# Kernel tuning notes

Measured on AMD Instinct MI355X. Metric: run time of the kernel, lower is better.

The kernel has to match this reference:

```python
import jax, jax.numpy as jnp
import numpy as np

NUM_BUCKETS = 32
MAX_DISTANCE = 128
NUM_HEADS = 16
D_KV = 64


def _relative_position_bucket(relative_position):
    # bidirectional buckets, faithful to T5Attention._relative_position_bucket
    num_buckets = NUM_BUCKETS // 2
    relative_buckets = (relative_position > 0).astype(jnp.int32) * num_buckets
    relative_position = jnp.abs(relative_position)
    max_exact = num_buckets // 2
    is_small = relative_position < max_exact
    rp_f = relative_position.astype(jnp.float32)
    rel_if_large = max_exact + (
        jnp.log(rp_f / max_exact) / np.log(MAX_DISTANCE / max_exact) * (num_buckets - max_exact)
    )
    rel_if_large = jnp.minimum(rel_if_large, num_buckets - 1)
    relative_buckets = relative_buckets + jnp.where(is_small, rp_f, rel_if_large).astype(jnp.int32)
    return relative_buckets


def setup_inputs() -> dict:
    key = jax.random.key(0)
    ks = jax.random.split(key, 6)
    B, S, D = 2, 2048, 1024
    inner = NUM_HEADS * D_KV  # 1024
    q_std = (inner * D_KV) ** (-0.5)
    kv_std = inner ** (-0.5)
    return {
        "hidden_states": jax.random.normal(ks[0], (B, S, D), jnp.float32),
        "attention_mask": jnp.ones((B, S), jnp.int32),
        "Wq": jax.random.normal(ks[1], (D, inner), jnp.float32) * q_std,
        "Wk": jax.random.normal(ks[2], (D, inner), jnp.float32) * kv_std,
        "Wv": jax.random.normal(ks[3], (D, inner), jnp.float32) * kv_std,
        "Wo": jax.random.normal(ks[4], (inner, D), jnp.float32) * kv_std,
        "rel_bias": jax.random.normal(ks[5], (NUM_BUCKETS, NUM_HEADS), jnp.float32),
    }


def reference(hidden_states, attention_mask, Wq, Wk, Wv, Wo, rel_bias):
    B, S, D = hidden_states.shape
    H, Dk = NUM_HEADS, D_KV

    q = (hidden_states @ Wq).reshape(B, S, H, Dk)
    k = (hidden_states @ Wk).reshape(B, S, H, Dk)
    v = (hidden_states @ Wv).reshape(B, S, H, Dk)
    q = q / jnp.sqrt(jnp.asarray(Dk, q.dtype))

    scores = jnp.einsum('bthd,bshd->bhts', q, k)  # [B,H,S,S]

    # relative position bias
    pos = jnp.arange(S, dtype=jnp.int32)
    rel_pos = pos[None, :] - pos[:, None]          # memory - context, [S,S]
    buckets = _relative_position_bucket(rel_pos)   # [S,S]
    bias = rel_bias[buckets]                       # [S,S,H]
    scores = scores + bias.transpose(2, 0, 1)[None].astype(scores.dtype)

    mask = attention_mask[:, None, None, :].astype(scores.dtype)
    scores = scores + (1.0 - mask) * jnp.finfo(scores.dtype).min

    attn = jax.nn.softmax(scores, axis=-1)
    out = jnp.einsum('bhts,bshd->bthd', attn, v).reshape(B, S, H * Dk)
    return out @ Wo
```

## Files before the change

kernel.cpp:

```cpp
#include <hip/hip_runtime.h>
#include <hip/hip_bf16.h>
#include <math.h>

typedef __attribute__((ext_vector_type(8))) short bf16x8;
typedef __attribute__((ext_vector_type(4))) short s16x4;
typedef __attribute__((ext_vector_type(4))) float f32x4;

constexpr int cB = 2, cS = 2048, cH = 16, cD = 64, cIn = 1024, cM = 1024;
constexpr float cLog2e = 1.4426950408889634f;

union BfPack { bf16x8 v; short s[8]; };
union BfPack4 { s16x4 v; short s[4]; };

__device__ __forceinline__ short f2bf(float f) {
    union { float f; unsigned u; } v; v.f = f;
    unsigned r = v.u + 0x7fffu + ((v.u >> 16) & 1u);
    return (short)(r >> 16);
}

__device__ __forceinline__ f32x4 mfma16(bf16x8 a, bf16x8 b, f32x4 c) {
    return __builtin_amdgcn_mfma_f32_16x16x32_bf16(a, b, c, 0, 0, 0);
}

__device__ __forceinline__ void async16(const short* g, short* l) {
    __builtin_amdgcn_global_load_lds(
        (const __attribute__((address_space(1))) unsigned*)(uintptr_t)g,
        (__attribute__((address_space(3))) unsigned*)(uintptr_t)l, 16, 0, 0);
}

__global__ __launch_bounds__(256) void prep_kernel(
    const float* __restrict__ hidden, short* __restrict__ hbf,
    const float* __restrict__ Wq, const float* __restrict__ Wk,
    const float* __restrict__ Wv, const float* __restrict__ Wo,
    short* __restrict__ Wt,
    const float* __restrict__ rel_bias, const int* __restrict__ mask,
    float* __restrict__ bt, float* __restrict__ maskadd) {
    const int bid = blockIdx.x;
    const int tid = threadIdx.x;
    if (bid < 2048) {
        int t = bid * 256 + tid;
        const float4* src = (const float4*)hidden;
        float4 a = src[2 * t], b = src[2 * t + 1];
        BfPack p;
        p.s[0] = f2bf(a.x); p.s[1] = f2bf(a.y); p.s[2] = f2bf(a.z); p.s[3] = f2bf(a.w);
        p.s[4] = f2bf(b.x); p.s[5] = f2bf(b.y); p.s[6] = f2bf(b.z); p.s[7] = f2bf(b.w);
        ((bf16x8*)hbf)[t] = p.v;
    } else if (bid < 3072) {
        const int b2 = bid - 2048;
        const int z = b2 >> 8, rem = b2 & 255;
        const float* W = (z == 0) ? Wq : (z == 1) ? Wk : (z == 2) ? Wv : Wo;
        const float scale = (z == 0) ? 0.125f * cLog2e : 1.0f;
        const int n0 = (rem & 15) * 64, k0 = (rem >> 4) * 64;
        __shared__ short sW[64][72];
        const int r = tid >> 2, c4 = (tid & 3) * 16;
        {
            const float* src = W + (size_t)(k0 + r) * cM + n0 + c4;
            BfPack p[2];
            #pragma unroll
            for (int q = 0; q < 2; q++) {
                float4 x = ((const float4*)src)[2 * q];
                float4 y = ((const float4*)src)[2 * q + 1];
                p[q].s[0] = f2bf(x.x * scale); p[q].s[1] = f2bf(x.y * scale);
                p[q].s[2] = f2bf(x.z * scale); p[q].s[3] = f2bf(x.w * scale);
                p[q].s[4] = f2bf(y.x * scale); p[q].s[5] = f2bf(y.y * scale);
                p[q].s[6] = f2bf(y.z * scale); p[q].s[7] = f2bf(y.w * scale);
            }
            *(bf16x8*)&sW[r][c4] = p[0].v;
            *(bf16x8*)&sW[r][c4 + 8] = p[1].v;
        }
        __syncthreads();
        const int n = tid >> 2, kc = (tid & 3) * 16;
        BfPack o0, o1;
        #pragma unroll
        for (int j = 0; j < 8; j++) o0.s[j] = sW[kc + j][n];
        #pragma unroll
        for (int j = 0; j < 8; j++) o1.s[j] = sW[kc + 8 + j][n];
        short* dst = Wt + (size_t)z * cM * cIn + (size_t)(n0 + n) * cIn + k0 + kc;
        *(bf16x8*)dst = o0.v;
        *(bf16x8*)(dst + 8) = o1.v;
    } else {
        int idx = (bid - 3072) * 256 + tid;
        if (idx < 4096) maskadd[idx] = (1.0f - (float)mask[idx]) * -3.0e38f;
        if (idx >= 4095) return;
        int delta = idx - 2047;
        int rb = (delta > 0) ? 16 : 0;
        int ar = delta < 0 ? -delta : delta;
        int bucket;
        if (ar < 8) {
            bucket = rb + ar;
        } else {
            float rl = 8.0f + logf((float)ar * 0.125f) * 2.8853900817779268f;
            rl = fminf(rl, 15.0f);
            bucket = rb + (int)rl;
        }
        #pragma unroll
        for (int h = 0; h < cH; h++)
            bt[h * 4096 + 2048 + delta] = rel_bias[bucket * cH + h] * cLog2e;
    }
}

template <bool SWAP>
__device__ __forceinline__ void gemm_core(
    const short* __restrict__ A, const short* __restrict__ Bt,
    short* smem, int m0, int c0, int tid, f32x4 (&acc)[4][4]) {
    const int w = tid >> 6, l = tid & 63;
    const int m16 = l & 15, g = l >> 4;
    const int srow = l >> 2, scol = (l & 3) * 8;
    const int mq = (w & 1) * 64, nq = (w >> 1) * 64;

    const short* pA0 = A + (size_t)(m0 + w * 16 + srow) * cIn + scol;
    const short* pA1 = A + (size_t)(m0 + 64 + w * 16 + srow) * cIn + scol;
    const short* pB0 = Bt + (size_t)(c0 + w * 16 + srow) * cIn + scol;
    const short* pB1 = Bt + (size_t)(c0 + 64 + w * 16 + srow) * cIn + scol;
    const int dof = w * 512 + l * 8;

    async16(pA0, smem + dof);
    async16(pA1, smem + 2048 + dof);
    async16(pB0, smem + 4096 + dof);
    async16(pB1, smem + 6144 + dof);
    __syncthreads();

    for (int k0 = 0; k0 < cIn; k0 += 32) {
        const int buf = (k0 >> 5) & 1;
        if (k0 + 32 < cIn) {
            short* dn = smem + (buf ^ 1) * 8192 + dof;
            async16(pA0 + k0 + 32, dn);
            async16(pA1 + k0 + 32, dn + 2048);
            async16(pB0 + k0 + 32, dn + 4096);
            async16(pB1 + k0 + 32, dn + 6144);
        }
        const short* sA = smem + buf * 8192;
        const short* sB = sA + 4096;
        bf16x8 af[4], bf[4];
        #pragma unroll
        for (int i = 0; i < 4; i++)
            af[i] = *(const bf16x8*)(sA + (mq + i * 16 + m16) * 32 + g * 8);
        #pragma unroll
        for (int j = 0; j < 4; j++)
            bf[j] = *(const bf16x8*)(sB + (nq + j * 16 + m16) * 32 + g * 8);
        #pragma unroll
        for (int i = 0; i < 4; i++)
            #pragma unroll
            for (int j = 0; j < 4; j++)
                acc[i][j] = SWAP ? mfma16(bf[j], af[i], acc[i][j])
                                 : mfma16(af[i], bf[j], acc[i][j]);
        __syncthreads();
    }
}

__global__ __launch_bounds__(256) void gemm_qkv_kernel(
    const short* __restrict__ hbf, const short* __restrict__ Wt,
    short* __restrict__ Qrm, short* __restrict__ Krm, short* __restrict__ VT) {
    const int raw = blockIdx.x;
    const int xcd = raw & 7;
    const int rest = raw >> 3;
    const int cblk = rest & 7;
    const int t = rest >> 3;
    const int z = t >> 2;
    const int m0 = (xcd * 4 + (t & 3)) * 128;
    const int c0 = cblk * 128;

    const short* Bt = Wt + (size_t)z * cM * cIn;
    __shared__ short smem[128 * 132];
    const int tid = threadIdx.x, w = tid >> 6, l = tid & 63;
    const int m16 = l & 15, g = l >> 4;
    const int mq = (w & 1) * 64, nq = (w >> 1) * 64;
    f32x4 acc[4][4] = {};

    if (z <= 1) {
        gemm_core<false>(hbf, Bt, smem, m0, c0, tid, acc);
        __syncthreads();
        #pragma unroll
        for (int i = 0; i < 4; i++)
            #pragma unroll
            for (int j = 0; j < 4; j++)
                #pragma unroll
                for (int r = 0; r < 4; r++)
                    smem[(mq + i * 16 + g * 4 + r) * 132 + nq + j * 16 + m16] =
                        f2bf(acc[i][j][r]);
        __syncthreads();
        const int tr = tid >> 1, hf = (tid & 1) * 64;
        short* dst = ((z == 0) ? Qrm : Krm) + (size_t)(m0 + tr) * cM + c0 + hf;
        #pragma unroll
        for (int c = 0; c < 8; c++)
            *(bf16x8*)(dst + c * 8) = *(const bf16x8*)(smem + tr * 132 + hf + c * 8);
    } else {
        gemm_core<true>(hbf, Bt, smem, m0, c0, tid, acc);
        __syncthreads();
        #pragma unroll
        for (int i = 0; i < 4; i++) {
            const int sl = mq + i * 16 + m16;
            const int s6 = sl & 63;
            const int pcol = (sl & 64) +
                             ((s6 & 3) | ((s6 & 28) << 1) | ((s6 >> 3) & 4));
            #pragma unroll
            for (int j = 0; j < 4; j++)
                #pragma unroll
                for (int r = 0; r < 4; r++)
                    smem[(nq + j * 16 + g * 4 + r) * 132 + pcol] =
                        f2bf(acc[i][j][r]);
        }
        __syncthreads();
        const int tr = tid >> 1, hf = (tid & 1) * 64;
        const int wcol = c0 + tr;
        short* dst = VT + (((size_t)(m0 >> 11) * cH + (wcol >> 6)) * cD +
                           (wcol & 63)) * cS + (m0 & 2047) + hf;
        #pragma unroll
        for (int c = 0; c < 8; c++)
            *(bf16x8*)(dst + c * 8) = *(const bf16x8*)(smem + tr * 132 + hf + c * 8);
    }
}

__global__ __launch_bounds__(512, 1) void attn_kernel(
    const short* __restrict__ Qrm, const short* __restrict__ Krm,
    const short* __restrict__ VTK, const float* __restrict__ maskadd,
    const float* __restrict__ bias_t, short* __restrict__ ctx) {
    const int raw = blockIdx.x;
    const int xcd = raw & 7, j = raw >> 3;
    const int qi = j & 7, grp = j >> 3;
    const int bh = grp * 8 + xcd;
    const int b = bh >> 4, h = bh & 15;
    const int q0 = qi * 256;

    const short* VTp = VTK + ((size_t)b * cH + h) * cS * cD;
    const float* mp = maskadd + b * cS;

    const int tid = threadIdx.x;
    const int wave = tid >> 6, lane = tid & 63;
    const int m16 = lane & 15, g = lane >> 4;

    __shared__ short Kt[2][128 * 64];
    __shared__ short Vt[2][64 * 128];
    __shared__ float bias_lds[2304];

    {
        const float* bw = bias_t + h * 4096 + 2048 - (q0 + 255);
        for (int i = tid; i < 2303; i += 512)
            bias_lds[i] = bw[i];
    }

    int qv[2];
    bf16x8 qf[2][2];
    #pragma unroll
    for (int qq = 0; qq < 2; qq++) {
        qv[qq] = q0 + wave * 16 + qq * 128 + m16;
        const short* qb = Qrm + (size_t)(b * cS + qv[qq]) * cM + h * cD;
        qf[qq][0] = *(const bf16x8*)(qb + g * 8);
        qf[qq][1] = *(const bf16x8*)(qb + 32 + g * 8);
    }

    int ib[2];
    #pragma unroll
    for (int qq = 0; qq < 2; qq++)
        ib[qq] = q0 + 255 + g * 4 - qv[qq];

    f32x4 o[2][4] = {};
    f32x4 lacc[2] = {};
    BfPack ones;
    #pragma unroll
    for (int i = 0; i < 8; i++) ones.s[i] = (short)0x3F80;

    const int u8 = tid & 7, r8 = tid >> 3;
    const int u16s = tid & 15, r16 = tid >> 4;
    const short* pK = Krm + ((size_t)b * cS + r8) * cM + h * cD +
                      ((u8 ^ (r8 & 7)) << 3);
    const short* pV = VTp + (size_t)r16 * cS + ((u16s ^ (r16 & 7)) << 3);
    short* dK = (short*)Kt + tid * 8;
    short* dV = (short*)Vt + tid * 8;

    const int kx0 = ((g ^ (m16 & 7)) << 3);
    const int kx1 = (((g + 4) ^ (m16 & 7)) << 3);

    #pragma unroll
    for (int c = 0; c < 2; c++) {
        async16(pK + (size_t)(c * 64) * cM, dK + c * 4096);
        async16(pV + (size_t)(c * 32) * cS, dV + c * 4096);
    }
    __syncthreads();

    for (int kt = 0; kt < cS; kt += 128) {
        const int buf = (kt >> 7) & 1, nxt = buf ^ 1;
        if (kt + 128 < cS) {
            #pragma unroll
            for (int c = 0; c < 2; c++) {
                async16(pK + (size_t)(kt + 128 + c * 64) * cM,
                        dK + nxt * 8192 + c * 4096);
                async16(pV + (size_t)(c * 32) * cS + kt + 128,
                        dV + nxt * 8192 + c * 4096);
            }
        }
        const short* K_ = (const short*)Kt + buf * 8192;
        const short* V_ = (const short*)Vt + buf * 8192;
        const int iq0 = ib[0] + kt, iq1 = ib[1] + kt;

        #pragma unroll
        for (int h2 = 0; h2 < 2; h2++) {
            f32x4 binit[2][4];
            #pragma unroll
            for (int t4 = 0; t4 < 4; t4++) {
                const int sto = (h2 * 4 + t4) * 16;
                f32x4 mk = *(const f32x4*)(mp + kt + sto + g * 4);
                #pragma unroll
                for (int c = 0; c < 4; c++) {
                    binit[0][t4][c] = bias_lds[iq0 + sto + c] + mk[c];
                    binit[1][t4][c] = bias_lds[iq1 + sto + c] + mk[c];
                }
            }

            f32x4 s[2][4];
            __builtin_amdgcn_s_setprio(1);
            #pragma unroll
            for (int t4 = 0; t4 < 4; t4++) {
                const int st = h2 * 4 + t4;
                bf16x8 klo = *(const bf16x8*)(K_ + (st * 16 + m16) * 64 + kx0);
                bf16x8 khi = *(const bf16x8*)(K_ + (st * 16 + m16) * 64 + kx1);
                #pragma unroll
                for (int qq = 0; qq < 2; qq++) {
                    f32x4 z4 = {};
                    s[qq][t4] = mfma16(khi, qf[qq][1],
                                       mfma16(klo, qf[qq][0], z4));
                }
            }
            __builtin_amdgcn_s_setprio(0);

            BfPack pp[2][2];
            #pragma unroll
            for (int qq = 0; qq < 2; qq++)
                #pragma unroll
                for (int t4 = 0; t4 < 4; t4++)
                    #pragma unroll
                    for (int r = 0; r < 2; r++) {
                        float p0 = __builtin_amdgcn_exp2f(s[qq][t4][2 * r] +
                                                          binit[qq][t4][2 * r]);
                        float p1 = __builtin_amdgcn_exp2f(s[qq][t4][2 * r + 1] +
                                                          binit[qq][t4][2 * r + 1]);
                        __hip_bfloat162 h2v = __float22bfloat162_rn(float2{p0, p1});
                        short2 sp = *(short2*)&h2v;
                        pp[qq][t4 & 1].s[(t4 >> 1) * 4 + 2 * r]     = sp.x;
                        pp[qq][t4 & 1].s[(t4 >> 1) * 4 + 2 * r + 1] = sp.y;
                    }

            __builtin_amdgcn_s_setprio(1);
            #pragma unroll
            for (int qq = 0; qq < 2; qq++) {
                lacc[qq] = mfma16(ones.v, pp[qq][0].v, lacc[qq]);
                lacc[qq] = mfma16(ones.v, pp[qq][1].v, lacc[qq]);
            }
            #pragma unroll
            for (int nt = 0; nt < 4; nt++) {
                bf16x8 vlo = *(const bf16x8*)(V_ + (nt * 16 + m16) * 128 +
                                              h2 * 64 + kx0);
                bf16x8 vhi = *(const bf16x8*)(V_ + (nt * 16 + m16) * 128 +
                                              h2 * 64 + kx1);
                #pragma unroll
                for (int qq = 0; qq < 2; qq++) {
                    o[qq][nt] = mfma16(vlo, pp[qq][0].v, o[qq][nt]);
                    o[qq][nt] = mfma16(vhi, pp[qq][1].v, o[qq][nt]);
                }
            }
            __builtin_amdgcn_s_setprio(0);
        }

        __syncthreads();
    }

    #pragma unroll
    for (int qq = 0; qq < 2; qq++) {
        const float inv = 1.0f / lacc[qq][0];
        short* cb = ctx + (size_t)(b * cS + qv[qq]) * cM + h * cD;
        #pragma unroll
        for (int nt = 0; nt < 4; nt++) {
            BfPack4 pk;
            #pragma unroll
            for (int r = 0; r < 4; r++) pk.s[r] = f2bf(o[qq][nt][r] * inv);
            *(s16x4*)(cb + nt * 16 + g * 4) = pk.v;
        }
    }
}

__global__ __launch_bounds__(256) void gemm_o_kernel(
    const short* __restrict__ ctx, const short* __restrict__ WoT,
    float* __restrict__ out) {
    const int raw = blockIdx.x;
    const int xcd = raw & 7;
    const int rest = raw >> 3;
    const int cblk = rest & 7;
    const int m0 = (xcd * 8 + (rest >> 3)) * 64;
    const int c0 = cblk * 128;

    __shared__ short smem[12288];
    const int tid = threadIdx.x, w = tid >> 6, l = tid & 63;
    const int m16 = l & 15, g = l >> 4;
    const int wm = (w & 1) * 32, wn = (w >> 1) * 64;
    const int sr = tid >> 2, sc = (tid & 3) * 8;
    f32x4 acc[2][4] = {};

    const short* pA = ctx + (size_t)(m0 + sr) * cIn + sc;
    const short* pB0 = WoT + (size_t)(c0 + sr) * cIn + sc;
    const short* pB1 = WoT + (size_t)(c0 + 64 + sr) * cIn + sc;

    async16(pA, smem + tid * 8);
    async16(pB0, smem + 2048 + tid * 8);
    async16(pB1, smem + 4096 + tid * 8);
    __syncthreads();

    for (int k0 = 0; k0 < cIn; k0 += 32) {
        const int buf = (k0 >> 5) & 1;
        if (k0 + 32 < cIn) {
            short* dn = smem + (buf ^ 1) * 6144 + tid * 8;
            async16(pA + k0 + 32, dn);
            async16(pB0 + k0 + 32, dn + 2048);
            async16(pB1 + k0 + 32, dn + 4096);
        }
        const short* sA = smem + buf * 6144;
        const short* sB = sA + 2048;
        bf16x8 af[2], bf[4];
        #pragma unroll
        for (int i = 0; i < 2; i++)
            af[i] = *(const bf16x8*)(sA + (wm + i * 16 + m16) * 32 + g * 8);
        #pragma unroll
        for (int jj = 0; jj < 4; jj++)
            bf[jj] = *(const bf16x8*)(sB + (wn + jj * 16 + m16) * 32 + g * 8);
        #pragma unroll
        for (int i = 0; i < 2; i++)
            #pragma unroll
            for (int jj = 0; jj < 4; jj++)
                acc[i][jj] = mfma16(af[i], bf[jj], acc[i][jj]);
        __syncthreads();
    }
    #pragma unroll
    for (int i = 0; i < 2; i++)
        #pragma unroll
        for (int jj = 0; jj < 4; jj++)
            #pragma unroll
            for (int r = 0; r < 4; r++)
                out[(size_t)(m0 + wm + i * 16 + g * 4 + r) * cM +
                    c0 + wn + jj * 16 + m16] = acc[i][jj][r];
}

extern "C" void kernel_launch(void* const* d_in, const int* in_sizes, int n_in,
                              void* d_out, int out_size, void* d_ws, size_t ws_size,
                              hipStream_t stream) {
    const float* hidden   = (const float*)d_in[0];
    const int*   mask     = (const int*)d_in[1];
    const float* Wq       = (const float*)d_in[2];
    const float* Wk       = (const float*)d_in[3];
    const float* Wv       = (const float*)d_in[4];
    const float* Wo       = (const float*)d_in[5];
    const float* rel_bias = (const float*)d_in[6];
    float* out = (float*)d_out;

    short* hbf_ctx = (short*)d_ws;
    short* Wt  = hbf_ctx + (size_t)4 * 1024 * 1024;
    short* Qrm = Wt  + (size_t)4 * 1024 * 1024;
    short* Krm = Qrm + (size_t)4 * 1024 * 1024;
    short* VT  = Krm + (size_t)4 * 1024 * 1024;
    float* bias_t  = (float*)(VT + (size_t)4 * 1024 * 1024);
    float* maskf   = bias_t + 16 * 4096;

    prep_kernel<<<3088, 256, 0, stream>>>(hidden, hbf_ctx, Wq, Wk, Wv, Wo, Wt,
                                          rel_bias, mask, bias_t, maskf);
    gemm_qkv_kernel<<<768, 256, 0, stream>>>(hbf_ctx, Wt, Qrm, Krm, VT);
    attn_kernel<<<256, 512, 0, stream>>>(Qrm, Krm, VT, maskf, bias_t, hbf_ctx);
    gemm_o_kernel<<<512, 256, 0, stream>>>(hbf_ctx, Wt + (size_t)3 * 1024 * 1024,
                                           out);
}
```

Measured before the change: 189.7 us.

## Shrink QKV GEMM tiles, stage mask in LDS, fold bias into MFMA accumulator

The QKV projection GEMM moves from 128x128 tiles with 768 blocks to 64x128 tiles with 1536 blocks. The XCD-aware block remapping is dropped and the epilogue is rewritten for the smaller tile. The attention kernel now copies the additive mask into LDS once per block instead of reading it from global memory in the inner loop. It also seeds the QK MFMA accumulator with bias plus mask, which removes the adds before exp2. Smaller GEMM tiles give more parallelism but less data reuse per block and lose the XCD-locality mapping.

```diff
diff --git a/kernel.cpp b/kernel.cpp
--- a/kernel.cpp
+++ b/kernel.cpp
@@ -99,115 +99,93 @@
     }
 }
 
-template <bool SWAP>
-__device__ __forceinline__ void gemm_core(
-    const short* __restrict__ A, const short* __restrict__ Bt,
-    short* smem, int m0, int c0, int tid, f32x4 (&acc)[4][4]) {
-    const int w = tid >> 6, l = tid & 63;
+__global__ __launch_bounds__(256) void gemm_qkv_kernel(
+    const short* __restrict__ hbf, const short* __restrict__ Wt,
+    short* __restrict__ Qrm, short* __restrict__ Krm, short* __restrict__ VT) {
+    const int bid = blockIdx.x;
+    const int z = bid >> 9;
+    const int rem = bid & 511;
+    const int m0 = (rem & 63) * 64;
+    const int c0 = (rem >> 6) * 128;
+    const short* Bt = Wt + (size_t)z * cM * cIn;
+
+    __shared__ short smem[12288];
+    const int tid = threadIdx.x, w = tid >> 6, l = tid & 63;
     const int m16 = l & 15, g = l >> 4;
-    const int srow = l >> 2, scol = (l & 3) * 8;
-    const int mq = (w & 1) * 64, nq = (w >> 1) * 64;
-
-    const short* pA0 = A + (size_t)(m0 + w * 16 + srow) * cIn + scol;
-    const short* pA1 = A + (size_t)(m0 + 64 + w * 16 + srow) * cIn + scol;
-    const short* pB0 = Bt + (size_t)(c0 + w * 16 + srow) * cIn + scol;
-    const short* pB1 = Bt + (size_t)(c0 + 64 + w * 16 + srow) * cIn + scol;
-    const int dof = w * 512 + l * 8;
-
-    async16(pA0, smem + dof);
-    async16(pA1, smem + 2048 + dof);
-    async16(pB0, smem + 4096 + dof);
-    async16(pB1, smem + 6144 + dof);
+    const int wm = (w & 1) * 32, wn = (w >> 1) * 64;
+    const int sr = tid >> 2, sc = (tid & 3) * 8;
+    f32x4 acc[2][4] = {};
+
+    const short* pA = hbf + (size_t)(m0 + sr) * cIn + sc;
+    const short* pB0 = Bt + (size_t)(c0 + sr) * cIn + sc;
+    const short* pB1 = Bt + (size_t)(c0 + 64 + sr) * cIn + sc;
+
+    async16(pA, smem + tid * 8);
+    async16(pB0, smem + 2048 + tid * 8);
+    async16(pB1, smem + 4096 + tid * 8);
     __syncthreads();
 
     for (int k0 = 0; k0 < cIn; k0 += 32) {
         const int buf = (k0 >> 5) & 1;
         if (k0 + 32 < cIn) {
-            short* dn = smem + (buf ^ 1) * 8192 + dof;
-            async16(pA0 + k0 + 32, dn);
-            async16(pA1 + k0 + 32, dn + 2048);
-            async16(pB0 + k0 + 32, dn + 4096);
-            async16(pB1 + k0 + 32, dn + 6144);
-        }
-        const short* sA = smem + buf * 8192;
-        const short* sB = sA + 4096;
-        bf16x8 af[4], bf[4];
-        #pragma unroll
-        for (int i = 0; i < 4; i++)
-            af[i] = *(const bf16x8*)(sA + (mq + i * 16 + m16) * 32 + g * 8);
-        #pragma unroll
-        for (int j = 0; j < 4; j++)
-            bf[j] = *(const bf16x8*)(sB + (nq + j * 16 + m16) * 32 + g * 8);
-        #pragma unroll
-        for (int i = 0; i < 4; i++)
-            #pragma unroll
-            for (int j = 0; j < 4; j++)
-                acc[i][j] = SWAP ? mfma16(bf[j], af[i], acc[i][j])
-                                 : mfma16(af[i], bf[j], acc[i][j]);
-        __syncthreads();
-    }
-}
-
-__global__ __launch_bounds__(256) void gemm_qkv_kernel(
-    const short* __restrict__ hbf, const short* __restrict__ Wt,
-    short* __restrict__ Qrm, short* __restrict__ Krm, short* __restrict__ VT) {
-    const int raw = blockIdx.x;
-    const int xcd = raw & 7;
-    const int rest = raw >> 3;
-    const int cblk = rest & 7;
-    const int t = rest >> 3;
-    const int z = t >> 2;
-    const int m0 = (xcd * 4 + (t & 3)) * 128;
-    const int c0 = cblk * 128;
-
-    const short* Bt = Wt + (size_t)z * cM * cIn;
-    __shared__ short smem[128 * 132];
-    const int tid = threadIdx.x, w = tid >> 6, l = tid & 63;
-    const int m16 = l & 15, g = l >> 4;
-    const int mq = (w & 1) * 64, nq = (w >> 1) * 64;
-    f32x4 acc[4][4] = {};
+            short* dn = smem + (buf ^ 1) * 6144 + tid * 8;
+            async16(pA + k0 + 32, dn);
+            async16(pB0 + k0 + 32, dn + 2048);
+            async16(pB1 + k0 + 32, dn + 4096);
+        }
+        const short* sA = smem + buf * 6144;
+        const short* sB = sA + 2048;
+        bf16x8 af[2], bf[4];
+        #pragma unroll
+        for (int i = 0; i < 2; i++)
+            af[i] = *(const bf16x8*)(sA + (wm + i * 16 + m16) * 32 + g * 8);
+        #pragma unroll
+        for (int jj = 0; jj < 4; jj++)
+            bf[jj] = *(const bf16x8*)(sB + (wn + jj * 16 + m16) * 32 + g * 8);
+        #pragma unroll
+        for (int i = 0; i < 2; i++)
+            #pragma unroll
+            for (int jj = 0; jj < 4; jj++)
+                acc[i][jj] = (z == 2) ? mfma16(bf[jj], af[i], acc[i][jj])
+                                      : mfma16(af[i], bf[jj], acc[i][jj]);
+        __syncthreads();
+    }
 
     if (z <= 1) {
-        gemm_core<false>(hbf, Bt, smem, m0, c0, tid, acc);
-        __syncthreads();
-        #pragma unroll
-        for (int i = 0; i < 4; i++)
-            #pragma unroll
-            for (int j = 0; j < 4; j++)
+        #pragma unroll
+        for (int i = 0; i < 2; i++)
+            #pragma unroll
+            for (int jj = 0; jj < 4; jj++)
                 #pragma unroll
                 for (int r = 0; r < 4; r++)
-                    smem[(mq + i * 16 + g * 4 + r) * 132 + nq + j * 16 + m16] =
-                        f2bf(acc[i][j][r]);
-        __syncthreads();
-        const int tr = tid >> 1, hf = (tid & 1) * 64;
+                    smem[(wm + i * 16 + g * 4 + r) * 132 + wn + jj * 16 + m16] =
+                        f2bf(acc[i][jj][r]);
+        __syncthreads();
+        const int tr = tid >> 2, hf = (tid & 3) * 32;
         short* dst = ((z == 0) ? Qrm : Krm) + (size_t)(m0 + tr) * cM + c0 + hf;
         #pragma unroll
-        for (int c = 0; c < 8; c++)
+        for (int c = 0; c < 4; c++)
             *(bf16x8*)(dst + c * 8) = *(const bf16x8*)(smem + tr * 132 + hf + c * 8);
     } else {
-        gemm_core<true>(hbf, Bt, smem, m0, c0, tid, acc);
-        __syncthreads();
-        #pragma unroll
-        for (int i = 0; i < 4; i++) {
-            const int sl = mq + i * 16 + m16;
-            const int s6 = sl & 63;
-            const int pcol = (sl & 64) +
-                             ((s6 & 3) | ((s6 & 28) << 1) | ((s6 >> 3) & 4));
-            #pragma unroll
-            for (int j = 0; j < 4; j++)
+        #pragma unroll
+        for (int i = 0; i < 2; i++) {
+            const int sl = wm + i * 16 + m16;
+            const int pcol = (sl & 3) | ((sl & 28) << 1) | ((sl >> 3) & 4);
+            #pragma unroll
+            for (int jj = 0; jj < 4; jj++)
                 #pragma unroll
                 for (int r = 0; r < 4; r++)
-                    smem[(nq + j * 16 + g * 4 + r) * 132 + pcol] =
-                        f2bf(acc[i][j][r]);
-        }
-        __syncthreads();
-        const int tr = tid >> 1, hf = (tid & 1) * 64;
+                    smem[(wn + jj * 16 + g * 4 + r) * 68 + pcol] =
+                        f2bf(acc[i][jj][r]);
+        }
+        __syncthreads();
+        const int tr = tid >> 1, hf = (tid & 1) * 32;
         const int wcol = c0 + tr;
         short* dst = VT + (((size_t)(m0 >> 11) * cH + (wcol >> 6)) * cD +
                            (wcol & 63)) * cS + (m0 & 2047) + hf;
         #pragma unroll
-        for (int c = 0; c < 8; c++)
-            *(bf16x8*)(dst + c * 8) = *(const bf16x8*)(smem + tr * 132 + hf + c * 8);
+        for (int c = 0; c < 4; c++)
+            *(bf16x8*)(dst + c * 8) = *(const bf16x8*)(smem + tr * 68 + hf + c * 8);
     }
 }
 
@@ -232,11 +210,13 @@
     __shared__ short Kt[2][128 * 64];
     __shared__ short Vt[2][64 * 128];
     __shared__ float bias_lds[2304];
+    __shared__ float mask_lds[2048];
 
     {
         const float* bw = bias_t + h * 4096 + 2048 - (q0 + 255);
         for (int i = tid; i < 2303; i += 512)
             bias_lds[i] = bw[i];
+        ((f32x4*)mask_lds)[tid & 511] = ((const f32x4*)mp)[tid & 511];
     }
 
     int qv[2];
@@ -299,7 +279,7 @@
             #pragma unroll
             for (int t4 = 0; t4 < 4; t4++) {
                 const int sto = (h2 * 4 + t4) * 16;
-                f32x4 mk = *(const f32x4*)(mp + kt + sto + g * 4);
+                f32x4 mk = *(const f32x4*)(mask_lds + kt + sto + g * 4);
                 #pragma unroll
                 for (int c = 0; c < 4; c++) {
                     binit[0][t4][c] = bias_lds[iq0 + sto + c] + mk[c];
@@ -315,11 +295,9 @@
                 bf16x8 klo = *(const bf16x8*)(K_ + (st * 16 + m16) * 64 + kx0);
                 bf16x8 khi = *(const bf16x8*)(K_ + (st * 16 + m16) * 64 + kx1);
                 #pragma unroll
-                for (int qq = 0; qq < 2; qq++) {
-                    f32x4 z4 = {};
+                for (int qq = 0; qq < 2; qq++)
                     s[qq][t4] = mfma16(khi, qf[qq][1],
-                                       mfma16(klo, qf[qq][0], z4));
-                }
+                                       mfma16(klo, qf[qq][0], binit[qq][t4]));
             }
             __builtin_amdgcn_s_setprio(0);
 
@@ -330,10 +308,8 @@
                 for (int t4 = 0; t4 < 4; t4++)
                     #pragma unroll
                     for (int r = 0; r < 2; r++) {
-                        float p0 = __builtin_amdgcn_exp2f(s[qq][t4][2 * r] +
-                                                          binit[qq][t4][2 * r]);
-                        float p1 = __builtin_amdgcn_exp2f(s[qq][t4][2 * r + 1] +
-                                                          binit[qq][t4][2 * r + 1]);
+                        float p0 = __builtin_amdgcn_exp2f(s[qq][t4][2 * r]);
+                        float p1 = __builtin_amdgcn_exp2f(s[qq][t4][2 * r + 1]);
                         __hip_bfloat162 h2v = __float22bfloat162_rn(float2{p0, p1});
                         short2 sp = *(short2*)&h2v;
                         pp[qq][t4 & 1].s[(t4 >> 1) * 4 + 2 * r]     = sp.x;
@@ -460,7 +436,7 @@
 
     prep_kernel<<<3088, 256, 0, stream>>>(hidden, hbf_ctx, Wq, Wk, Wv, Wo, Wt,
                                           rel_bias, mask, bias_t, maskf);
-    gemm_qkv_kernel<<<768, 256, 0, stream>>>(hbf_ctx, Wt, Qrm, Krm, VT);
+    gemm_qkv_kernel<<<1536, 256, 0, stream>>>(hbf_ctx, Wt, Qrm, Krm, VT);
     attn_kernel<<<256, 512, 0, stream>>>(Qrm, Krm, VT, maskf, bias_t, hbf_ctx);
     gemm_o_kernel<<<512, 256, 0, stream>>>(hbf_ctx, Wt + (size_t)3 * 1024 * 1024,
                                            out);
```

After: 195.7 us. 1.03x slower.
